# Optimization experiments

Measured on AMD Instinct MI355X. Metric: run time of the kernel, lower is better.

Reference implementation:

```python
import jax, jax.numpy as jnp
import numpy as np

K = 16  # K_neighbors

def linear_positions(pixels):
    # normalized flat (pixels, 2) grid positions, matching LinearPositions(normalize=True, flat_output=True)
    wd = int(round(pixels ** 0.5))
    h = jnp.repeat(jnp.arange(wd, dtype=jnp.float32)[:, None], wd, axis=1)
    w = jnp.repeat(jnp.arange(wd, dtype=jnp.float32)[None, :], wd, axis=0)
    pos = jnp.stack([h, w], axis=-1) / (wd - 1)
    return pos.reshape(pixels, 2)


def setup_inputs() -> dict:
    key = jax.random.key(0)
    ks = jax.random.split(key, 8)
    B, Wn, P, C = 4, 16, 256, 32
    inp = {
        "x": jax.random.normal(ks[0], (B, Wn, P, C), dtype=jnp.float32),
        "sf_w0": jax.random.normal(ks[1], (3 * K, 128), dtype=jnp.float32) * 0.05,
        "sf_b0": jnp.zeros((128,), jnp.float32),
        "sf_w1": jax.random.normal(ks[2], (128, 128), dtype=jnp.float32) * 0.05,
        "sf_b1": jnp.zeros((128,), jnp.float32),
        "sf_wo": jax.random.normal(ks[3], (128, 64), dtype=jnp.float32) * 0.05,
        "sf_bo": jnp.zeros((64,), jnp.float32),
        "out_w0": jax.random.normal(ks[4], (C + 64, 128), dtype=jnp.float32) * 0.05,
        "out_b0": jnp.zeros((128,), jnp.float32),
        "out_w1": jax.random.normal(ks[5], (128, 128), dtype=jnp.float32) * 0.05,
        "out_b1": jnp.zeros((128,), jnp.float32),
        "out_wo": jax.random.normal(ks[6], (128, 64), dtype=jnp.float32) * 0.05,
        "out_bo": jnp.zeros((64,), jnp.float32),
    }
    return inp


def reference(x, sf_w0, sf_b0, sf_w1, sf_b1, sf_wo, sf_bo,
              out_w0, out_b0, out_w1, out_b1, out_wo, out_bo):
    B, Wn, P, C = x.shape
    # L1 similarity: 1 - mean |x_i - x_j| over channels -> (B, Wn, P, P)
    w = 1.0 - jnp.mean(jnp.abs(x[:, :, :, None, :] - x[:, :, None, :, :]), axis=-1)
    K_scores, K_idxs = jax.lax.top_k(w, K)  # (B, Wn, P, K)
    pos = linear_positions(P)  # (P, 2)
    # source pos for pixel i minus gathered target pos of its K neighbors
    rel = pos[None, None, :, None, :] - pos[K_idxs]  # (B, Wn, P, K, 2)
    K_rel_pos = rel.reshape(B, Wn, P, K * 2)
    # sf FFN
    h = jnp.concatenate([K_scores, K_rel_pos], axis=-1)  # (B, Wn, P, 3K)
    h = jax.nn.relu(h @ sf_w0 + sf_b0)
    h = jax.nn.relu(h @ sf_w1 + sf_b1)
    sf = h @ sf_wo + sf_bo  # (B, Wn, P, 64)
    # out FFN
    h = jnp.concatenate([x, sf], axis=-1)  # (B, Wn, P, C+64)
    h = jax.nn.relu(h @ out_w0 + out_b0)
    h = jax.nn.relu(h @ out_w1 + out_b1)
    return h @ out_wo + out_bo  # (B, Wn, P, 64)
```

## Files before the change

### kernel.cpp

```cpp
#include <hip/hip_runtime.h>
#include <hip/hip_bf16.h>

#define K_SEL 16
#define NCAND 20

typedef __attribute__((ext_vector_type(8))) short short8;
typedef __attribute__((ext_vector_type(4))) short short4v;
typedef __attribute__((ext_vector_type(4))) float f32x4;

__device__ __forceinline__ short f2bf_bits(float v) {
    union { __hip_bfloat16 b; short s; } u;
    u.b = __float2bfloat16(v);
    return u.s;
}
__device__ __forceinline__ float bf2f_bits(short h) {
    return __uint_as_float(((unsigned)(unsigned short)h) << 16);
}

__global__ __launch_bounds__(1024) void simtopk_kernel(
    const float* __restrict__ x,
    float* __restrict__ feat)
{
    __shared__ __align__(16) float xsT[8192];
    __shared__ int    candj[16][NCAND];
    __shared__ double rs[16][NCAND];

    const int tid  = threadIdx.x;
    const int win  = blockIdx.x >> 4;
    const int grp  = blockIdx.x & 15;
    const int lane = tid & 63;
    const int wv   = tid >> 6;

    if (tid < 512) {
        const int c4 = tid & 7, jb = tid >> 3;
        const float4* gx = reinterpret_cast<const float4*>(x + (size_t)win * 8192);
        float4 v0 = gx[jb * 8 + c4];
        float4 v1 = gx[jb * 8 + c4 + 512];
        float4 v2 = gx[jb * 8 + c4 + 1024];
        float4 v3 = gx[jb * 8 + c4 + 1536];
        float4* xsT4 = reinterpret_cast<float4*>(xsT);
        const int gsw = jb ^ c4;
        xsT4[(4 * c4 + 0) * 64 + gsw] = make_float4(v0.x, v1.x, v2.x, v3.x);
        xsT4[(4 * c4 + 1) * 64 + gsw] = make_float4(v0.y, v1.y, v2.y, v3.y);
        xsT4[(4 * c4 + 2) * 64 + gsw] = make_float4(v0.z, v1.z, v2.z, v3.z);
        xsT4[(4 * c4 + 3) * 64 + gsw] = make_float4(v0.w, v1.w, v2.w, v3.w);
    }

    const int iu = __builtin_amdgcn_readfirstlane(grp * 16 + wv);
    const float* xrow = x + (size_t)win * 8192 + (size_t)iu * 32;
    float xi[32];
    #pragma unroll
    for (int c = 0; c < 32; ++c) xi[c] = xrow[c];

    __syncthreads();

    const float4* xsT4c = reinterpret_cast<const float4*>(xsT);
    float a0 = 0.f, a1 = 0.f, a2 = 0.f, a3 = 0.f;
    #pragma unroll
    for (int c = 0; c < 32; ++c) {
        float4 a = xsT4c[c * 64 + (lane ^ ((c >> 2) & 7))];
        a0 += fabsf(a.x - xi[c]);
        a1 += fabsf(a.y - xi[c]);
        a2 += fabsf(a.z - xi[c]);
        a3 += fabsf(a.w - xi[c]);
    }
    unsigned int p[4];
    p[0] = (__float_as_uint(a0) & 0xFFFFFF00u) | (unsigned)(lane);
    p[1] = (__float_as_uint(a1) & 0xFFFFFF00u) | (unsigned)(lane + 64);
    p[2] = (__float_as_uint(a2) & 0xFFFFFF00u) | (unsigned)(lane + 128);
    p[3] = (__float_as_uint(a3) & 0xFFFFFF00u) | (unsigned)(lane + 192);

    unsigned int T = 0;
    for (int bit = 31; bit >= 0; --bit) {
        unsigned int cand = T | (1u << bit);
        int cnt = __popcll(__ballot(p[0] < cand)) + __popcll(__ballot(p[1] < cand))
                + __popcll(__ballot(p[2] < cand)) + __popcll(__ballot(p[3] < cand));
        if (cnt < NCAND) T = cand;
    }

    const unsigned long long lt = (1ull << lane) - 1ull;
    int base = 0;
    #pragma unroll
    for (int q = 0; q < 4; ++q) {
        bool sel = (p[q] <= T);
        unsigned long long m = __ballot(sel);
        if (sel) candj[wv][base + __popcll(m & lt)] = q * 64 + lane;
        base += __popcll(m);
    }
    asm volatile("s_waitcnt lgkmcnt(0)" ::: "memory");

    double s = 0.0;
    int myj = -1;
    if (lane < NCAND) {
        myj = candj[wv][lane];
        const int jl = myj & 63, jq = myj >> 6;
        #pragma unroll
        for (int c = 0; c < 32; ++c) {
            float bv = xsT[(c * 64 + (jl ^ ((c >> 2) & 7))) * 4 + jq];
            s += fabs((double)xi[c] - (double)bv);
        }
        rs[wv][lane] = s;
    }
    asm volatile("s_waitcnt lgkmcnt(0)" ::: "memory");

    if (myj >= 0) {
        int rank = 0;
        #pragma unroll 4
        for (int o = 0; o < NCAND; ++o) {
            double so = rs[wv][o];
            int    jo = candj[wv][o];
            rank += (so < s || (so == s && jo < myj)) ? 1 : 0;
        }
        if (rank < K_SEL) {
            const int gp = win * 256 + iu;
            feat[gp * 48 + rank] = (float)(1.0 - s * 0.03125);
            float dh = (float)((iu >> 4) - (myj >> 4)) * (1.0f / 15.0f);
            float dw = (float)((iu & 15) - (myj & 15)) * (1.0f / 15.0f);
            reinterpret_cast<float2*>(feat)[gp * 24 + 8 + rank] = make_float2(dh, dw);
        }
    }
}

__global__ __launch_bounds__(256) void pack_kernel(
    const float* __restrict__ s0w, const float* __restrict__ s1w,
    const float* __restrict__ sow, const float* __restrict__ o0w,
    const float* __restrict__ o1w, const float* __restrict__ oow,
    short* __restrict__ wpack)
{
    int t = blockIdx.x * 256 + threadIdx.x;
    if (t >= 69632) return;
    int l, base;
    if      (t <  8192) { l = 0; base = 0;     }
    else if (t < 24576) { l = 1; base = 8192;  }
    else if (t < 32768) { l = 2; base = 24576; }
    else if (t < 45056) { l = 3; base = 32768; }
    else if (t < 61440) { l = 4; base = 45056; }
    else                { l = 5; base = 61440; }

    const float* W = (l == 0) ? s0w : (l == 1) ? s1w : (l == 2) ? sow
                   : (l == 3) ? o0w : (l == 4) ? o1w : oow;
    int N    = (l == 2 || l == 5) ? 64 : 128;
    int Kr   = (l == 0) ? 48 : (l == 3) ? 96 : 128;
    int woff = (l == 0) ? 0 : (l == 1) ? 16384 : (l == 2) ? 49152
             : (l == 3) ? 65536 : (l == 4) ? 90112 : 122880;
    int sz   = (l == 2 || l == 5) ? 8192 : (l == 3) ? 12288 : (l == 0) ? 8192 : 16384;

    int e = t - base;
    int i = e & 7, kb = (e >> 3) & 3, rem = e >> 5;
    int n = rem % N, ks = rem / N;
    int k = ks * 32 + kb * 8 + i;
    float v = (k < Kr) ? W[k * N + n] : 0.0f;
    short hi = f2bf_bits(v);
    float lo = v - bf2f_bits(hi);
    wpack[woff + e]      = hi;
    wpack[woff + sz + e] = f2bf_bits(lo);
}

template<int K_STEPS, int N, bool RELU, bool TO_GLOBAL>
__device__ __forceinline__ void bf16_layer(
    const short* hiIn, const short* loIn, short* hiOut, short* loOut,
    float* gout, int pbase, const short* __restrict__ wpack, int woff, int sz,
    const float* __restrict__ bias, int wv, int lane, int out_col_off)
{
    if (N == 64 && wv >= 8) return;
    const int mt  = wv & 1;
    const int nt  = wv >> 1;
    const int m_a = mt * 16 + (lane & 15);
    const int kb  = lane >> 4;
    const int n   = nt * 16 + (lane & 15);

    f32x4 acc = (f32x4){0.f, 0.f, 0.f, 0.f};
    #pragma unroll
    for (int ks = 0; ks < K_STEPS; ++ks) {
        const int g   = ks * 4 + kb;
        const int off = m_a * 256 + ((g ^ (m_a & 7)) << 4);
        short8 ahi = *(const short8*)((const char*)hiIn + off);
        short8 alo = *(const short8*)((const char*)loIn + off);
        const int wi = woff + ((ks * N + n) * 4 + kb) * 8;
        short8 whi = *(const short8*)(wpack + wi);
        short8 wlo = *(const short8*)(wpack + wi + sz);
        acc = __builtin_amdgcn_mfma_f32_16x16x32_bf16(ahi, whi, acc, 0, 0, 0);
        acc = __builtin_amdgcn_mfma_f32_16x16x32_bf16(ahi, wlo, acc, 0, 0, 0);
        acc = __builtin_amdgcn_mfma_f32_16x16x32_bf16(alo, whi, acc, 0, 0, 0);
    }

    const float bv = bias[n];
    #pragma unroll
    for (int r = 0; r < 4; ++r) {
        float v = acc[r] + bv;
        if (RELU) v = fmaxf(v, 0.0f);
        const int pw = mt * 16 + (lane >> 4) * 4 + r;
        if (TO_GLOBAL) {
            gout[(size_t)(pbase + pw) * 64 + n] = v;
        } else {
            const int w   = out_col_off + n;
            const int off = pw * 256 + ((((w >> 3) ^ (pw & 7))) << 4) + (w & 7) * 2;
            short h = f2bf_bits(v);
            short l = f2bf_bits(v - bf2f_bits(h));
            *(short*)((char*)hiOut + off) = h;
            *(short*)((char*)loOut + off) = l;
        }
    }
}

__global__ __launch_bounds__(1024) void ffn_kernel(
    const float* __restrict__ x,
    const float* __restrict__ feat,
    const short* __restrict__ wpack,
    const float* __restrict__ s0b, const float* __restrict__ s1b,
    const float* __restrict__ sob, const float* __restrict__ o0b,
    const float* __restrict__ o1b, const float* __restrict__ oob,
    float* __restrict__ out)
{
    __shared__ __align__(16) short hiA[32 * 128];
    __shared__ __align__(16) short loA[32 * 128];
    __shared__ __align__(16) short hiB[32 * 128];
    __shared__ __align__(16) short loB[32 * 128];

    const int tid   = threadIdx.x;
    const int lane  = tid & 63;
    const int wv    = tid >> 6;
    const int pbase = blockIdx.x * 32;

    if (tid < 384) {
        int p = tid / 12, c4 = tid - p * 12;
        f32x4 v = ((const f32x4*)feat)[(size_t)(pbase + p) * 12 + c4];
        short4v h4, l4;
        #pragma unroll
        for (int j = 0; j < 4; ++j) {
            short h = f2bf_bits(v[j]);
            h4[j] = h;
            l4[j] = f2bf_bits(v[j] - bf2f_bits(h));
        }
        int off = p * 256 + ((((c4 >> 1) ^ (p & 7))) << 4) + (c4 & 1) * 8;
        *(short4v*)((char*)hiA + off) = h4;
        *(short4v*)((char*)loA + off) = l4;
    } else if (tid < 512) {
        int t2 = tid - 384;
        int p = t2 & 31, sel = t2 >> 5;
        int g = 6 + (sel & 1);
        int off = p * 256 + ((g ^ (p & 7)) << 4);
        short8 z = (short8){0,0,0,0,0,0,0,0};
        if (sel >> 1) *(short8*)((char*)loA + off) = z;
        else          *(short8*)((char*)hiA + off) = z;
    }
    __syncthreads();

    bf16_layer<2, 128, true, false>(hiA, loA, hiB, loB, nullptr, pbase,
                                    wpack, 0, 8192, s0b, wv, lane, 0);
    __syncthreads();
    bf16_layer<4, 128, true, false>(hiB, loB, hiA, loA, nullptr, pbase,
                                    wpack, 16384, 16384, s1b, wv, lane, 0);
    __syncthreads();
    if (tid < 256) {
        int p = tid >> 3, c4 = tid & 7;
        f32x4 v = ((const f32x4*)x)[(size_t)(pbase + p) * 8 + c4];
        short4v h4, l4;
        #pragma unroll
        for (int j = 0; j < 4; ++j) {
            short h = f2bf_bits(v[j]);
            h4[j] = h;
            l4[j] = f2bf_bits(v[j] - bf2f_bits(h));
        }
        int off = p * 256 + ((((c4 >> 1) ^ (p & 7))) << 4) + (c4 & 1) * 8;
        *(short4v*)((char*)hiB + off) = h4;
        *(short4v*)((char*)loB + off) = l4;
    }
    bf16_layer<4, 64, false, false>(hiA, loA, hiB, loB, nullptr, pbase,
                                    wpack, 49152, 8192, sob, wv, lane, 32);
    __syncthreads();
    bf16_layer<3, 128, true, false>(hiB, loB, hiA, loA, nullptr, pbase,
                                    wpack, 65536, 12288, o0b, wv, lane, 0);
    __syncthreads();
    bf16_layer<4, 128, true, false>(hiA, loA, hiB, loB, nullptr, pbase,
                                    wpack, 90112, 16384, o1b, wv, lane, 0);
    __syncthreads();
    bf16_layer<4, 64, false, true>(hiB, loB, nullptr, nullptr, out, pbase,
                                   wpack, 122880, 8192, oob, wv, lane, 0);
}

extern "C" void kernel_launch(void* const* d_in, const int* in_sizes, int n_in,
                              void* d_out, int out_size, void* d_ws, size_t ws_size,
                              hipStream_t stream) {
    const float* x    = (const float*)d_in[0];
    const float* s0w  = (const float*)d_in[1];
    const float* s0b  = (const float*)d_in[2];
    const float* s1w  = (const float*)d_in[3];
    const float* s1b  = (const float*)d_in[4];
    const float* sow  = (const float*)d_in[5];
    const float* sob  = (const float*)d_in[6];
    const float* o0w  = (const float*)d_in[7];
    const float* o0b  = (const float*)d_in[8];
    const float* o1w  = (const float*)d_in[9];
    const float* o1b  = (const float*)d_in[10];
    const float* oow  = (const float*)d_in[11];
    const float* oob  = (const float*)d_in[12];

    short* wpack = (short*)d_ws;
    float* feat  = (float*)((char*)d_ws + 524288);
    float* out   = (float*)d_out;

    pack_kernel<<<272, 256, 0, stream>>>(s0w, s1w, sow, o0w, o1w, oow, wpack);
    simtopk_kernel<<<1024, 1024, 0, stream>>>(x, feat);
    ffn_kernel<<<512, 1024, 0, stream>>>(x, feat, wpack,
                                         s0b, s1b, sob, o0b, o1b, oob,
                                         out);
}
```

Measured before the change: 58.54 us.

## Process two query pixels per wavefront in similarity top-k kernel

Each wavefront now handles two query pixels instead of one, so the block count is halved and each staged window tile in shared memory serves twice as many queries. Query channel values are taken by readlane from the transposed shared tile instead of a per-lane global row load. The threshold bisection and candidate ranking run for both queries at once. The kernel is templated on which float4 component holds the query. This lowers the count of shared-memory staging passes and global loads, at the cost of more registers per thread and longer per-wave serial bisection work.

```diff
diff --git a/kernel.cpp b/kernel.cpp
--- a/kernel.cpp
+++ b/kernel.cpp
@@ -16,18 +16,15 @@
 __device__ __forceinline__ float bf2f_bits(short h) {
     return __uint_as_float(((unsigned)(unsigned short)h) << 16);
 }
-
-__global__ __launch_bounds__(1024) void simtopk_kernel(
-    const float* __restrict__ x,
-    float* __restrict__ feat)
-{
-    __shared__ __align__(16) float xsT[8192];
-    __shared__ int    candj[16][NCAND];
-    __shared__ double rs[16][NCAND];
-
-    const int tid  = threadIdx.x;
-    const int win  = blockIdx.x >> 4;
-    const int grp  = blockIdx.x & 15;
+__device__ __forceinline__ float readlane_f(float v, int l) {
+    return __int_as_float(__builtin_amdgcn_readlane(__float_as_int(v), l));
+}
+
+template<int COMP>
+__device__ __forceinline__ void simtopk_body(
+    const float* __restrict__ x, float* __restrict__ feat,
+    float* xsT, int* candj, double* rs, int win, int grp, int tid)
+{
     const int lane = tid & 63;
     const int wv   = tid >> 6;
 
@@ -45,79 +42,111 @@
         xsT4[(4 * c4 + 2) * 64 + gsw] = make_float4(v0.z, v1.z, v2.z, v3.z);
         xsT4[(4 * c4 + 3) * 64 + gsw] = make_float4(v0.w, v1.w, v2.w, v3.w);
     }
-
-    const int iu = __builtin_amdgcn_readfirstlane(grp * 16 + wv);
-    const float* xrow = x + (size_t)win * 8192 + (size_t)iu * 32;
-    float xi[32];
-    #pragma unroll
-    for (int c = 0; c < 32; ++c) xi[c] = xrow[c];
-
-    __syncthreads();
-
-    const float4* xsT4c = reinterpret_cast<const float4*>(xsT);
-    float a0 = 0.f, a1 = 0.f, a2 = 0.f, a3 = 0.f;
+    __syncthreads();
+
+    const int plbase = (grp & 1) * 32 + wv * 2;
+
+    const f32x4* xsT4c = reinterpret_cast<const f32x4*>(xsT);
+    float acc0[4] = {0.f, 0.f, 0.f, 0.f};
+    float acc1[4] = {0.f, 0.f, 0.f, 0.f};
     #pragma unroll
     for (int c = 0; c < 32; ++c) {
-        float4 a = xsT4c[c * 64 + (lane ^ ((c >> 2) & 7))];
-        a0 += fabsf(a.x - xi[c]);
-        a1 += fabsf(a.y - xi[c]);
-        a2 += fabsf(a.z - xi[c]);
-        a3 += fabsf(a.w - xi[c]);
-    }
-    unsigned int p[4];
-    p[0] = (__float_as_uint(a0) & 0xFFFFFF00u) | (unsigned)(lane);
-    p[1] = (__float_as_uint(a1) & 0xFFFFFF00u) | (unsigned)(lane + 64);
-    p[2] = (__float_as_uint(a2) & 0xFFFFFF00u) | (unsigned)(lane + 128);
-    p[3] = (__float_as_uint(a3) & 0xFFFFFF00u) | (unsigned)(lane + 192);
-
-    unsigned int T = 0;
+        f32x4 a = xsT4c[c * 64 + (lane ^ ((c >> 2) & 7))];
+        float xi0 = readlane_f(a[COMP], plbase);
+        float xi1 = readlane_f(a[COMP], plbase + 1);
+        #pragma unroll
+        for (int q = 0; q < 4; ++q) {
+            acc0[q] += fabsf(a[q] - xi0);
+            acc1[q] += fabsf(a[q] - xi1);
+        }
+    }
+    unsigned int p0[4], p1[4];
+    #pragma unroll
+    for (int q = 0; q < 4; ++q) {
+        p0[q] = (__float_as_uint(acc0[q]) & 0xFFFFFF00u) | (unsigned)(q * 64 + lane);
+        p1[q] = (__float_as_uint(acc1[q]) & 0xFFFFFF00u) | (unsigned)(q * 64 + lane);
+    }
+
+    unsigned int T0 = 0, T1 = 0;
     for (int bit = 31; bit >= 0; --bit) {
-        unsigned int cand = T | (1u << bit);
-        int cnt = __popcll(__ballot(p[0] < cand)) + __popcll(__ballot(p[1] < cand))
-                + __popcll(__ballot(p[2] < cand)) + __popcll(__ballot(p[3] < cand));
-        if (cnt < NCAND) T = cand;
+        unsigned int c0 = T0 | (1u << bit), c1 = T1 | (1u << bit);
+        int n0 = __popcll(__ballot(p0[0] < c0)) + __popcll(__ballot(p0[1] < c0))
+               + __popcll(__ballot(p0[2] < c0)) + __popcll(__ballot(p0[3] < c0));
+        int n1 = __popcll(__ballot(p1[0] < c1)) + __popcll(__ballot(p1[1] < c1))
+               + __popcll(__ballot(p1[2] < c1)) + __popcll(__ballot(p1[3] < c1));
+        if (n0 < NCAND) T0 = c0;
+        if (n1 < NCAND) T1 = c1;
     }
 
     const unsigned long long lt = (1ull << lane) - 1ull;
-    int base = 0;
+    int base0 = 0, base1 = 0;
     #pragma unroll
     for (int q = 0; q < 4; ++q) {
-        bool sel = (p[q] <= T);
-        unsigned long long m = __ballot(sel);
-        if (sel) candj[wv][base + __popcll(m & lt)] = q * 64 + lane;
-        base += __popcll(m);
+        bool s0 = (p0[q] <= T0);
+        unsigned long long m0 = __ballot(s0);
+        if (s0) candj[(wv * 2 + 0) * NCAND + base0 + __popcll(m0 & lt)] = q * 64 + lane;
+        base0 += __popcll(m0);
+        bool s1 = (p1[q] <= T1);
+        unsigned long long m1 = __ballot(s1);
+        if (s1) candj[(wv * 2 + 1) * NCAND + base1 + __popcll(m1 & lt)] = q * 64 + lane;
+        base1 += __popcll(m1);
     }
     asm volatile("s_waitcnt lgkmcnt(0)" ::: "memory");
 
+    const int t  = lane >> 5;
+    const int cl = lane & 31;
     double s = 0.0;
     int myj = -1;
-    if (lane < NCAND) {
-        myj = candj[wv][lane];
+    if (cl < NCAND) {
+        myj = candj[(wv * 2 + t) * NCAND + cl];
         const int jl = myj & 63, jq = myj >> 6;
+        const int pl = plbase + t;
         #pragma unroll
         for (int c = 0; c < 32; ++c) {
-            float bv = xsT[(c * 64 + (jl ^ ((c >> 2) & 7))) * 4 + jq];
-            s += fabs((double)xi[c] - (double)bv);
-        }
-        rs[wv][lane] = s;
+            float xiv = xsT[(c * 64 + (pl ^ ((c >> 2) & 7))) * 4 + COMP];
+            float bv  = xsT[(c * 64 + (jl ^ ((c >> 2) & 7))) * 4 + jq];
+            s += fabs((double)xiv - (double)bv);
+        }
+        rs[(wv * 2 + t) * NCAND + cl] = s;
     }
     asm volatile("s_waitcnt lgkmcnt(0)" ::: "memory");
 
-    if (myj >= 0) {
+    if (cl < NCAND) {
         int rank = 0;
         #pragma unroll 4
         for (int o = 0; o < NCAND; ++o) {
-            double so = rs[wv][o];
-            int    jo = candj[wv][o];
+            double so = rs[(wv * 2 + t) * NCAND + o];
+            int    jo = candj[(wv * 2 + t) * NCAND + o];
             rank += (so < s || (so == s && jo < myj)) ? 1 : 0;
         }
         if (rank < K_SEL) {
-            const int gp = win * 256 + iu;
+            const int pwin = grp * 32 + wv * 2 + t;
+            const int gp   = win * 256 + pwin;
             feat[gp * 48 + rank] = (float)(1.0 - s * 0.03125);
-            float dh = (float)((iu >> 4) - (myj >> 4)) * (1.0f / 15.0f);
-            float dw = (float)((iu & 15) - (myj & 15)) * (1.0f / 15.0f);
+            float dh = (float)((pwin >> 4) - (myj >> 4)) * (1.0f / 15.0f);
+            float dw = (float)((pwin & 15) - (myj & 15)) * (1.0f / 15.0f);
             reinterpret_cast<float2*>(feat)[gp * 24 + 8 + rank] = make_float2(dh, dw);
         }
+    }
+}
+
+__global__ __launch_bounds__(1024) void simtopk_kernel(
+    const float* __restrict__ x,
+    float* __restrict__ feat)
+{
+    __shared__ __align__(16) float xsT[8192];
+    __shared__ int    candj[16 * 2 * NCAND];
+    __shared__ double rs[16 * 2 * NCAND];
+
+    const int tid = threadIdx.x;
+    const int win = blockIdx.x >> 3;
+    const int grp = blockIdx.x & 7;
+
+    switch (grp >> 1) {
+        case 0: simtopk_body<0>(x, feat, xsT, candj, rs, win, grp, tid); break;
+        case 1: simtopk_body<1>(x, feat, xsT, candj, rs, win, grp, tid); break;
+        case 2: simtopk_body<2>(x, feat, xsT, candj, rs, win, grp, tid); break;
+        default: simtopk_body<3>(x, feat, xsT, candj, rs, win, grp, tid); break;
     }
 }
 
@@ -301,7 +330,7 @@
     float* out   = (float*)d_out;
 
     pack_kernel<<<272, 256, 0, stream>>>(s0w, s1w, sow, o0w, o1w, oow, wpack);
-    simtopk_kernel<<<1024, 1024, 0, stream>>>(x, feat);
+    simtopk_kernel<<<512, 1024, 0, stream>>>(x, feat);
     ffn_kernel<<<512, 1024, 0, stream>>>(x, feat, wpack,
                                          s0b, s1b, sob, o0b, o1b, oob,
                                          out);
```

New measurement: 52.98 us. 9.5% less time.
